# Kernel optimization log

Measured on AMD Instinct MI355X. Metric: run time of the kernel, lower is better.

The kernel has to match this reference:

```python
import jax, jax.numpy as jnp
import numpy as np

N_NODES = 32
GAT_OUT = 64
LSTM_H = 128
N_CLS = 4
NEG_SLOPE = 0.2


def setup_inputs() -> dict:
    key = jax.random.key(0)
    ks = jax.random.split(key, 12)
    B, T, E = 32, 512, 96
    F, H = GAT_OUT, LSTM_H
    s = 0.05
    return {
        "x_seq": jax.random.normal(ks[0], (B, T, N_NODES), jnp.float32),
        "edge_index": jax.random.randint(ks[1], (2, E), 0, N_NODES, jnp.int32),
        # GATConv params (heads=1): lin weight [in=1, F], attention vectors [F], bias [F]
        "w_gat": jax.random.normal(ks[2], (1, F), jnp.float32) * s,
        "att_src": jax.random.normal(ks[3], (F,), jnp.float32) * s,
        "att_dst": jax.random.normal(ks[4], (F,), jnp.float32) * s,
        "b_gat": jnp.zeros((F,), jnp.float32),
        # LSTM params, torch gate order (i, f, g, o)
        "W_ih": jax.random.normal(ks[5], (N_NODES * F, 4 * H), jnp.float32) * s,
        "W_hh": jax.random.normal(ks[6], (H, 4 * H), jnp.float32) * s,
        "b_ih": jnp.zeros((4 * H,), jnp.float32),
        "b_hh": jnp.zeros((4 * H,), jnp.float32),
        # classifier
        "W_fc": jax.random.normal(ks[7], (H, N_CLS), jnp.float32) * s,
        "b_fc": jnp.zeros((N_CLS,), jnp.float32),
    }


def _forward(x_seq, edge_index, w_gat, att_src, att_dst, b_gat,
             W_ih, W_hh, b_ih, b_hh, W_fc, b_fc):
    B, T, N = x_seq.shape
    F = w_gat.shape[1]
    H = W_hh.shape[0]

    # --- GAT over all (B,T) steps at once (PyG GATConv, heads=1, self-loops) ---
    loops = jnp.arange(N, dtype=edge_index.dtype)
    src = jnp.concatenate([edge_index[0], loops])  # [Et]
    dst = jnp.concatenate([edge_index[1], loops])  # [Et]
    Et = src.shape[0]

    h = x_seq[..., None] * w_gat            # [B,T,N,F] (in_channels=1 linear)
    a_s = h @ att_src                        # [B,T,N]
    a_d = h @ att_dst                        # [B,T,N]
    e = a_s[..., src] + a_d[..., dst]        # [B,T,Et]
    e = jnp.where(e > 0, e, NEG_SLOPE * e)   # LeakyReLU(0.2)

    # segment softmax over destination node, batched over B*T
    e2 = jnp.moveaxis(e, -1, 0).reshape(Et, B * T)
    m = jax.ops.segment_max(e2, dst, num_segments=N)        # [N,B*T]
    ex = jnp.exp(e2 - m[dst])
    z = jax.ops.segment_sum(ex, dst, num_segments=N)        # [N,B*T]
    alpha = ex / z[dst]                                      # [Et,B*T]
    alpha = jnp.moveaxis(alpha.reshape(Et, B, T), 0, -1)     # [B,T,Et]

    msg = alpha[..., None] * h[:, :, src, :]                 # [B,T,Et,F]
    onehot = (dst[:, None] == jnp.arange(N)).astype(h.dtype)  # [Et,N]
    out = jnp.einsum('btef,en->btnf', msg, onehot) + b_gat    # [B,T,N,F]

    seq = out.reshape(B, T, N * F)           # [B,T,2048]

    # --- single-layer LSTM (batch_first), torch gate order i,f,g,o ---
    xw = seq @ W_ih + (b_ih + b_hh)          # [B,T,4H]

    def step(carry, xw_t):
        hs, cs = carry
        g = xw_t + hs @ W_hh                 # [B,4H]
        i, f, gg, o = jnp.split(g, 4, axis=-1)
        cs = jax.nn.sigmoid(f) * cs + jax.nn.sigmoid(i) * jnp.tanh(gg)
        hs = jax.nn.sigmoid(o) * jnp.tanh(cs)
        return (hs, cs), None

    h0 = jnp.zeros((B, H), seq.dtype)
    (h_last, _), _ = jax.lax.scan(step, (h0, h0), jnp.moveaxis(xw, 1, 0))

    return h_last @ W_fc + b_fc              # [B,num_classes]


def reference(x_seq, edge_index, w_gat, att_src, att_dst, b_gat,
              W_ih, W_hh, b_ih, b_hh, W_fc, b_fc):
    return _forward(x_seq, edge_index, w_gat, att_src, att_dst, b_gat,
                    W_ih, W_hh, b_ih, b_hh, W_fc, b_fc)
```

## Files before the change

kernel.cpp:

```cpp
#include <hip/hip_runtime.h>

#define NN 32
#define FF 64
#define HH 128
#define G4 512
#define BB 32
#define TT 512
#define ET 128
#define NPOS (BB*TT)
#define POSB 32

__device__ __forceinline__ float frcp(float x) { return __builtin_amdgcn_rcpf(x); }

__global__ __launch_bounds__(512) void prep_kernel(const float* __restrict__ w_gat,
                                                   const float* __restrict__ b_gat,
                                                   const float* __restrict__ W_ih,
                                                   const float* __restrict__ W_hh,
                                                   float* __restrict__ W_eff,
                                                   float* __restrict__ biasp,
                                                   float* __restrict__ Wt) {
  int j = threadIdx.x;
  int n = blockIdx.x;
  float accw = 0.f, accb = 0.f;
#pragma unroll 8
  for (int f = 0; f < FF; ++f) {
    float wv = W_ih[(n * FF + f) * G4 + j];
    accw = fmaf(w_gat[f], wv, accw);
    accb = fmaf(b_gat[f], wv, accb);
  }
  W_eff[n * G4 + j] = accw;
  biasp[n * G4 + j] = accb;
  int g0 = (n * G4 + j) * 4;
#pragma unroll
  for (int q = 0; q < 4; ++q) {
    int e = g0 + q;
    int tl = e >> 7, idx = e & 127;
    int r = tl >> 2, kq = tl & 3;
    int g = idx >> 5, kk = idx & 31;
    Wt[e] = W_hh[(kq * 32 + kk) * G4 + g * 128 + r];
  }
}

__global__ __launch_bounds__(256) void gatxw_kernel(const float* __restrict__ x_seq,
                                                    const int* __restrict__ ei,
                                                    const float* __restrict__ w_gat,
                                                    const float* __restrict__ att_src,
                                                    const float* __restrict__ att_dst,
                                                    const float* __restrict__ b_ih,
                                                    const float* __restrict__ b_hh,
                                                    const float* __restrict__ W_eff,
                                                    const float* __restrict__ biasp,
                                                    float* __restrict__ xw) {
  __shared__ int srt[ET];
  __shared__ int offs[NN + 1];
  __shared__ int cnt[NN];
  __shared__ float xs[POSB * NN];
  __shared__ float sl[POSB * NN];
  __shared__ float scal_sh[2];
  int tid = threadIdx.x;
  int posbase = blockIdx.x * POSB;
  float we0[NN], we1[NN];
#pragma unroll
  for (int nn = 0; nn < NN; ++nn) {
    we0[nn] = W_eff[nn * G4 + tid];
    we1[nn] = W_eff[nn * G4 + 256 + tid];
  }
  float b0 = b_ih[tid] + b_hh[tid];
  float b1 = b_ih[256 + tid] + b_hh[256 + tid];
#pragma unroll 8
  for (int n = 0; n < NN; ++n) {
    b0 += biasp[n * G4 + tid];
    b1 += biasp[n * G4 + 256 + tid];
  }
  if (tid < NN) cnt[tid] = 0;
  __syncthreads();
  int es = 0, ed = 0, tk = 0;
  if (tid < ET) {
    if (tid < 96) { es = ei[tid]; ed = ei[96 + tid]; }
    else { es = tid - 96; ed = tid - 96; }
    tk = atomicAdd(&cnt[ed], 1);
  }
  __syncthreads();
  if (tid == 0) {
    offs[0] = 0;
    for (int n = 0; n < NN; ++n) offs[n + 1] = offs[n] + cnt[n];
  }
  if (tid == 1) {
    float cs = 0.f, cd = 0.f;
    for (int f = 0; f < FF; ++f) {
      cs = fmaf(w_gat[f], att_src[f], cs);
      cd = fmaf(w_gat[f], att_dst[f], cd);
    }
    scal_sh[0] = cs;
    scal_sh[1] = cd;
  }
  __syncthreads();
  if (tid < ET) srt[offs[ed] + tk] = es;
#pragma unroll
  for (int c = 0; c < POSB * NN / 256; ++c)
    xs[c * 256 + tid] = x_seq[posbase * NN + c * 256 + tid];
  __syncthreads();
  float cs = scal_sh[0], cd = scal_sh[1];
  int n = tid & 31;
  int e0 = offs[n], e1 = offs[n + 1];
#pragma unroll
  for (int pb = 0; pb < POSB / 8; ++pb) {
    int p = pb * 8 + (tid >> 5);
    int base = p * 32;
    float xn = xs[base + n];
    float cdxn = cd * xn;
    float m = -3.0e38f;
    for (int e = e0; e < e1; ++e) {
      float ev = fmaf(cs, xs[base + srt[e]], cdxn);
      ev = ev > 0.f ? ev : 0.2f * ev;
      m = fmaxf(m, ev);
    }
    float z = 0.f, sa = 0.f;
    for (int e = e0; e < e1; ++e) {
      float xsv = xs[base + srt[e]];
      float ev = fmaf(cs, xsv, cdxn);
      ev = ev > 0.f ? ev : 0.2f * ev;
      float ex = __expf(ev - m);
      z += ex;
      sa = fmaf(ex, xsv, sa);
    }
    sl[base + n] = sa * frcp(z);
  }
  __syncthreads();
#pragma unroll 4
  for (int pp = 0; pp < POSB; ++pp) {
    const float4* sp = (const float4*)&sl[pp * 32];
    float a0 = b0, a1 = b1;
#pragma unroll
    for (int q = 0; q < 8; ++q) {
      float4 sv = sp[q];
      a0 = fmaf(sv.x, we0[4 * q], a0);
      a0 = fmaf(sv.y, we0[4 * q + 1], a0);
      a0 = fmaf(sv.z, we0[4 * q + 2], a0);
      a0 = fmaf(sv.w, we0[4 * q + 3], a0);
      a1 = fmaf(sv.x, we1[4 * q], a1);
      a1 = fmaf(sv.y, we1[4 * q + 1], a1);
      a1 = fmaf(sv.z, we1[4 * q + 2], a1);
      a1 = fmaf(sv.w, we1[4 * q + 3], a1);
    }
    size_t row = (size_t)(posbase + pp) * G4;
    xw[row + tid] = a0;
    xw[row + 256 + tid] = a1;
  }
}


#define PK16F(HP, W0, W1, W2, W3) \
  "v_pk_fma_f32 v[216:217], v[" HP "], v[" W0 "], 0\n\t" \
  "v_pk_fma_f32 v[218:219], v[" HP "], v[" W1 "], 0\n\t" \
  "v_pk_fma_f32 v[220:221], v[" HP "], v[" W2 "], 0\n\t" \
  "v_pk_fma_f32 v[222:223], v[" HP "], v[" W3 "], 0\n\t"

#define PK16A(HP, W0, W1, W2, W3) \
  "v_pk_fma_f32 v[216:217], v[" HP "], v[" W0 "], v[216:217]\n\t" \
  "v_pk_fma_f32 v[218:219], v[" HP "], v[" W1 "], v[218:219]\n\t" \
  "v_pk_fma_f32 v[220:221], v[" HP "], v[" W2 "], v[220:221]\n\t" \
  "v_pk_fma_f32 v[222:223], v[" HP "], v[" W3 "], v[222:223]\n\t"

#define PHASE(XSLOT, RD, WR) \
  "ds_read_b128 v[32:35], " RD "\n\t" \
  "ds_read_b128 v[36:39], " RD " offset:16\n\t" \
  "ds_read_b128 v[40:43], " RD " offset:32\n\t" \
  "ds_read_b128 v[44:47], " RD " offset:48\n\t" \
  "ds_read_b128 v[48:51], " RD " offset:64\n\t" \
  "ds_read_b128 v[52:55], " RD " offset:80\n\t" \
  "ds_read_b128 v[56:59], " RD " offset:96\n\t" \
  "ds_read_b128 v[60:63], " RD " offset:112\n\t" \
  "s_waitcnt lgkmcnt(7)\n\t" \
  PK16F("32:33", "64:65",  "96:97",   "128:129", "160:161") \
  PK16A("34:35", "66:67",  "98:99",   "130:131", "162:163") \
  "s_waitcnt lgkmcnt(6)\n\t" \
  PK16A("36:37", "68:69",  "100:101", "132:133", "164:165") \
  PK16A("38:39", "70:71",  "102:103", "134:135", "166:167") \
  "s_waitcnt lgkmcnt(5)\n\t" \
  PK16A("40:41", "72:73",  "104:105", "136:137", "168:169") \
  PK16A("42:43", "74:75",  "106:107", "138:139", "170:171") \
  "s_waitcnt lgkmcnt(4)\n\t" \
  PK16A("44:45", "76:77",  "108:109", "140:141", "172:173") \
  PK16A("46:47", "78:79",  "110:111", "142:143", "174:175") \
  "s_waitcnt lgkmcnt(3)\n\t" \
  PK16A("48:49", "80:81",  "112:113", "144:145", "176:177") \
  PK16A("50:51", "82:83",  "114:115", "146:147", "178:179") \
  "s_waitcnt lgkmcnt(2)\n\t" \
  PK16A("52:53", "84:85",  "116:117", "148:149", "180:181") \
  PK16A("54:55", "86:87",  "118:119", "150:151", "182:183") \
  "s_waitcnt lgkmcnt(1)\n\t" \
  PK16A("56:57", "88:89",  "120:121", "152:153", "184:185") \
  PK16A("58:59", "90:91",  "122:123", "154:155", "186:187") \
  "s_waitcnt lgkmcnt(0)\n\t" \
  PK16A("60:61", "92:93",  "124:125", "156:157", "188:189") \
  PK16A("62:63", "94:95",  "126:127", "158:159", "190:191") \
  "s_waitcnt vmcnt(3)\n\t" \
  "v_mov_b32 v215, " XSLOT "\n\t" \
  "global_load_dword " XSLOT ", v194, %[xwb]\n\t" \
  "v_add_u32 v194, 0x800, v194\n\t" \
  "v_add_f32 v204, v216, v217\n\t" \
  "v_add_f32 v205, v218, v219\n\t" \
  "v_add_f32 v206, v220, v221\n\t" \
  "v_add_f32 v207, v222, v223\n\t" \
  "v_add_f32_dpp v204, v204, v204 quad_perm:[1,0,3,2] row_mask:0xf bank_mask:0xf\n\t" \
  "v_add_f32_dpp v205, v205, v205 quad_perm:[1,0,3,2] row_mask:0xf bank_mask:0xf\n\t" \
  "v_add_f32_dpp v206, v206, v206 quad_perm:[1,0,3,2] row_mask:0xf bank_mask:0xf\n\t" \
  "v_add_f32_dpp v207, v207, v207 quad_perm:[1,0,3,2] row_mask:0xf bank_mask:0xf\n\t" \
  "v_add_f32_dpp v204, v204, v204 quad_perm:[2,3,0,1] row_mask:0xf bank_mask:0xf\n\t" \
  "v_add_f32_dpp v205, v205, v205 quad_perm:[2,3,0,1] row_mask:0xf bank_mask:0xf\n\t" \
  "v_add_f32_dpp v206, v206, v206 quad_perm:[2,3,0,1] row_mask:0xf bank_mask:0xf\n\t" \
  "v_add_f32_dpp v207, v207, v207 quad_perm:[2,3,0,1] row_mask:0xf bank_mask:0xf\n\t" \
  "v_cndmask_b32 v208, v204, v205, s[22:23]\n\t" \
  "v_cndmask_b32 v209, v206, v207, s[22:23]\n\t" \
  "v_cndmask_b32 v208, v208, v209, s[24:25]\n\t" \
  "v_add_f32 v208, v208, v215\n\t" \
  "v_mul_f32 v209, v200, v208\n\t" \
  "v_exp_f32 v209, v209\n\t" \
  "s_nop 0\n\t" \
  "v_add_f32 v209, 1.0, v209\n\t" \
  "v_rcp_f32 v209, v209\n\t" \
  "s_nop 0\n\t" \
  "v_fma_f32 v210, v201, v209, v202\n\t" \
  "s_nop 1\n\t" \
  "v_add_f32_dpp v211, v210, v203 quad_perm:[0,0,0,0] row_mask:0xf bank_mask:0xf\n\t" \
  "v_add_f32_dpp v212, v210, v203 quad_perm:[1,1,1,1] row_mask:0xf bank_mask:0xf\n\t" \
  "v_add_f32_dpp v213, v210, v203 quad_perm:[2,2,2,2] row_mask:0xf bank_mask:0xf\n\t" \
  "v_add_f32_dpp v214, v210, v203 quad_perm:[3,3,3,3] row_mask:0xf bank_mask:0xf\n\t" \
  "v_mul_f32 v211, v211, v213\n\t" \
  "v_fma_f32 v199, v212, v199, v211\n\t" \
  "v_mul_f32 v209, 0x4038aa3b, v199\n\t" \
  "v_exp_f32 v209, v209\n\t" \
  "s_nop 0\n\t" \
  "v_add_f32 v209, 1.0, v209\n\t" \
  "v_rcp_f32 v209, v209\n\t" \
  "s_nop 0\n\t" \
  "v_fma_f32 v209, -2.0, v209, 1.0\n\t" \
  "v_mul_f32 v209, v214, v209\n\t" \
  "ds_write_b32 " WR ", v209\n\t" \
  "s_waitcnt lgkmcnt(0)\n\t" \
  "s_barrier\n\t"

__global__ __launch_bounds__(512, 2) void lstm_kernel(const float* __restrict__ xw,
                                                      const float* __restrict__ Wt,
                                                      const float* __restrict__ W_fc,
                                                      const float* __restrict__ b_fc,
                                                      float* __restrict__ out) {
  __shared__ __align__(16) float lds[320];
  int b = blockIdx.x, tid = threadIdx.x;
  int r = tid >> 2, kq = tid & 3;
  if (tid < 320) lds[tid] = 0.f;
  const float* xwb = xw + (size_t)b * TT * G4;
  unsigned xoff0 = (unsigned)((kq * 128 + r) * 4);
  unsigned wtoff = (unsigned)(tid * 512);
  unsigned lbase = (unsigned)(uintptr_t)&lds[0];
  unsigned rda = lbase + kq * 160;
  unsigned rdb = rda + 640;
  unsigned wra = lbase + (((r >> 5) * 40 + (r & 31)) << 2);
  unsigned wrb = wra + 640;
  float kmulf = (kq == 2) ? __uint_as_float(0x4038aa3bu)
                          : __uint_as_float(0xbfb8aa3bu);
  float Af = (kq == 2) ? -2.f : 1.f;
  float Bf = (kq == 2) ? 1.f : 0.f;
  unsigned kqodd = kq & 1, kqhi = kq >> 1;
  __syncthreads();
  asm volatile(
    "v_mov_b32 v194, %[xo]\n\t"
    "v_mov_b32 v195, %[rda]\n\t"
    "v_mov_b32 v196, %[rdb]\n\t"
    "v_mov_b32 v197, %[wra]\n\t"
    "v_mov_b32 v198, %[wrb]\n\t"
    "v_mov_b32 v199, 0\n\t"
    "v_mov_b32 v200, %[km]\n\t"
    "v_mov_b32 v201, %[Aa]\n\t"
    "v_mov_b32 v202, %[Bb]\n\t"
    "v_mov_b32 v203, 0\n\t"
    "v_cmp_eq_u32 s[22:23], 1, %[kodd]\n\t"
    "v_cmp_eq_u32 s[24:25], 1, %[khi]\n\t"
    "global_load_dword v224, v194, %[xwb]\n\t"
    "v_add_u32 v194, 0x800, v194\n\t"
    "global_load_dword v225, v194, %[xwb]\n\t"
    "v_add_u32 v194, 0x800, v194\n\t"
    "global_load_dword v226, v194, %[xwb]\n\t"
    "v_add_u32 v194, 0x800, v194\n\t"
    "global_load_dword v227, v194, %[xwb]\n\t"
    "v_add_u32 v194, 0x800, v194\n\t"
    "global_load_dwordx4 v[64:67], %[wto], %[wtb] offset:0\n\t"
    "global_load_dwordx4 v[68:71], %[wto], %[wtb] offset:16\n\t"
    "global_load_dwordx4 v[72:75], %[wto], %[wtb] offset:32\n\t"
    "global_load_dwordx4 v[76:79], %[wto], %[wtb] offset:48\n\t"
    "global_load_dwordx4 v[80:83], %[wto], %[wtb] offset:64\n\t"
    "global_load_dwordx4 v[84:87], %[wto], %[wtb] offset:80\n\t"
    "global_load_dwordx4 v[88:91], %[wto], %[wtb] offset:96\n\t"
    "global_load_dwordx4 v[92:95], %[wto], %[wtb] offset:112\n\t"
    "global_load_dwordx4 v[96:99], %[wto], %[wtb] offset:128\n\t"
    "global_load_dwordx4 v[100:103], %[wto], %[wtb] offset:144\n\t"
    "global_load_dwordx4 v[104:107], %[wto], %[wtb] offset:160\n\t"
    "global_load_dwordx4 v[108:111], %[wto], %[wtb] offset:176\n\t"
    "global_load_dwordx4 v[112:115], %[wto], %[wtb] offset:192\n\t"
    "global_load_dwordx4 v[116:119], %[wto], %[wtb] offset:208\n\t"
    "global_load_dwordx4 v[120:123], %[wto], %[wtb] offset:224\n\t"
    "global_load_dwordx4 v[124:127], %[wto], %[wtb] offset:240\n\t"
    "global_load_dwordx4 v[128:131], %[wto], %[wtb] offset:256\n\t"
    "global_load_dwordx4 v[132:135], %[wto], %[wtb] offset:272\n\t"
    "global_load_dwordx4 v[136:139], %[wto], %[wtb] offset:288\n\t"
    "global_load_dwordx4 v[140:143], %[wto], %[wtb] offset:304\n\t"
    "global_load_dwordx4 v[144:147], %[wto], %[wtb] offset:320\n\t"
    "global_load_dwordx4 v[148:151], %[wto], %[wtb] offset:336\n\t"
    "global_load_dwordx4 v[152:155], %[wto], %[wtb] offset:352\n\t"
    "global_load_dwordx4 v[156:159], %[wto], %[wtb] offset:368\n\t"
    "global_load_dwordx4 v[160:163], %[wto], %[wtb] offset:384\n\t"
    "global_load_dwordx4 v[164:167], %[wto], %[wtb] offset:400\n\t"
    "global_load_dwordx4 v[168:171], %[wto], %[wtb] offset:416\n\t"
    "global_load_dwordx4 v[172:175], %[wto], %[wtb] offset:432\n\t"
    "global_load_dwordx4 v[176:179], %[wto], %[wtb] offset:448\n\t"
    "global_load_dwordx4 v[180:183], %[wto], %[wtb] offset:464\n\t"
    "global_load_dwordx4 v[184:187], %[wto], %[wtb] offset:480\n\t"
    "global_load_dwordx4 v[188:191], %[wto], %[wtb] offset:496\n\t"
    "s_waitcnt vmcnt(0)\n\t"
    "s_movk_i32 s20, 0x80\n\t"
    "L_lstm_%=:\n\t"
    PHASE("v224", "v195", "v198")
    PHASE("v225", "v196", "v197")
    PHASE("v226", "v195", "v198")
    PHASE("v227", "v196", "v197")
    "s_sub_u32 s20, s20, 1\n\t"
    "s_cmp_lg_u32 s20, 0\n\t"
    "s_cbranch_scc1 L_lstm_%=\n\t"
    "s_waitcnt vmcnt(0) lgkmcnt(0)\n\t"
    :
    : [xwb]"s"(xwb), [wtb]"s"(Wt), [wto]"v"(wtoff), [xo]"v"(xoff0),
      [rda]"v"(rda), [rdb]"v"(rdb), [wra]"v"(wra), [wrb]"v"(wrb),
      [km]"v"(kmulf), [Aa]"v"(Af), [Bb]"v"(Bf),
      [kodd]"v"(kqodd), [khi]"v"(kqhi)
    : "memory", "scc", "s20", "s22", "s23", "s24", "s25",
      "v32","v33","v34","v35","v36","v37","v38","v39",
      "v40","v41","v42","v43","v44","v45","v46","v47",
      "v48","v49","v50","v51","v52","v53","v54","v55",
      "v56","v57","v58","v59","v60","v61","v62","v63",
      "v64","v65","v66","v67","v68","v69","v70","v71",
      "v72","v73","v74","v75","v76","v77","v78","v79",
      "v80","v81","v82","v83","v84","v85","v86","v87",
      "v88","v89","v90","v91","v92","v93","v94","v95",
      "v96","v97","v98","v99","v100","v101","v102","v103",
      "v104","v105","v106","v107","v108","v109","v110","v111",
      "v112","v113","v114","v115","v116","v117","v118","v119",
      "v120","v121","v122","v123","v124","v125","v126","v127",
      "v128","v129","v130","v131","v132","v133","v134","v135",
      "v136","v137","v138","v139","v140","v141","v142","v143",
      "v144","v145","v146","v147","v148","v149","v150","v151",
      "v152","v153","v154","v155","v156","v157","v158","v159",
      "v160","v161","v162","v163","v164","v165","v166","v167",
      "v168","v169","v170","v171","v172","v173","v174","v175",
      "v176","v177","v178","v179","v180","v181","v182","v183",
      "v184","v185","v186","v187","v188","v189","v190","v191",
      "v192","v193","v194","v195","v196","v197","v198","v199",
      "v200","v201","v202","v203","v204","v205","v206","v207",
      "v208","v209","v210","v211","v212","v213","v214","v215",
      "v216","v217","v218","v219","v220","v221","v222","v223",
      "v224","v225","v226","v227");
  __syncthreads();
  if (tid < 4) {
    float acc = b_fc[tid];
#pragma unroll 8
    for (int k = 0; k < HH; ++k)
      acc = fmaf(lds[(k >> 5) * 40 + (k & 31)], W_fc[k * 4 + tid], acc);
    out[b * 4 + tid] = acc;
  }
}

extern "C" void kernel_launch(void* const* d_in, const int* in_sizes, int n_in,
                              void* d_out, int out_size, void* d_ws, size_t ws_size,
                              hipStream_t stream) {
  const float* x_seq   = (const float*)d_in[0];
  const int*   ei      = (const int*)d_in[1];
  const float* w_gat   = (const float*)d_in[2];
  const float* att_src = (const float*)d_in[3];
  const float* att_dst = (const float*)d_in[4];
  const float* b_gat   = (const float*)d_in[5];
  const float* W_ih    = (const float*)d_in[6];
  const float* W_hh    = (const float*)d_in[7];
  const float* b_ih    = (const float*)d_in[8];
  const float* b_hh    = (const float*)d_in[9];
  const float* W_fc    = (const float*)d_in[10];
  const float* b_fc    = (const float*)d_in[11];

  float* ws = (float*)d_ws;
  float* Wt    = ws;
  float* xw    = Wt + 65536;
  float* W_eff = xw + (size_t)(NPOS + 8) * G4;
  float* biasp = W_eff + NN * G4;

  prep_kernel<<<NN, G4, 0, stream>>>(w_gat, b_gat, W_ih, W_hh, W_eff, biasp, Wt);
  gatxw_kernel<<<NPOS / POSB, 256, 0, stream>>>(x_seq, ei, w_gat, att_src, att_dst,
                                                b_ih, b_hh, W_eff, biasp, xw);
  lstm_kernel<<<BB, G4, 0, stream>>>(xw, Wt, W_fc, b_fc, (float*)d_out);
}
```

Baseline: 374.7 us.

## Use fp16 dot2 for LSTM recurrent matvec with half-precision weights and hidden state

Stores the transposed W_hh in fp16, packed so that consecutive k pairs sit together, and stores the hidden state in LDS as fp16. The recurrent matvec then uses v_dot2_f32_f16 with fp32 accumulation in place of packed fp32 FMAs. This halves the per-step LDS reads and the register-resident weight footprint, and drops the pairwise add stage before the DPP reduction. The cost is lower precision in the recurrence over 512 steps, which risks numerical drift.

```diff
diff --git a/kernel.cpp b/kernel.cpp
--- a/kernel.cpp
+++ b/kernel.cpp
@@ -1,4 +1,5 @@
 #include <hip/hip_runtime.h>
+#include <hip/hip_fp16.h>
 
 #define NN 32
 #define FF 64
@@ -30,14 +31,18 @@
   }
   W_eff[n * G4 + j] = accw;
   biasp[n * G4 + j] = accb;
+  __half* Wt16 = (__half*)Wt;
   int g0 = (n * G4 + j) * 4;
 #pragma unroll
   for (int q = 0; q < 4; ++q) {
-    int e = g0 + q;
-    int tl = e >> 7, idx = e & 127;
+    int E = g0 + q;
+    int tl = E >> 7, idx = E & 127;
     int r = tl >> 2, kq = tl & 3;
-    int g = idx >> 5, kk = idx & 31;
-    Wt[e] = W_hh[(kq * 32 + kk) * G4 + g * 128 + r];
+    int P = idx >> 3;
+    int g = (idx >> 1) & 3;
+    int e = idx & 1;
+    int k = kq * 32 + 2 * P + e;
+    Wt16[E] = __float2half(W_hh[k * G4 + g * 128 + r]);
   }
 }
 
@@ -150,70 +155,58 @@
 }
 
 
-#define PK16F(HP, W0, W1, W2, W3) \
-  "v_pk_fma_f32 v[216:217], v[" HP "], v[" W0 "], 0\n\t" \
-  "v_pk_fma_f32 v[218:219], v[" HP "], v[" W1 "], 0\n\t" \
-  "v_pk_fma_f32 v[220:221], v[" HP "], v[" W2 "], 0\n\t" \
-  "v_pk_fma_f32 v[222:223], v[" HP "], v[" W3 "], 0\n\t"
-
-#define PK16A(HP, W0, W1, W2, W3) \
-  "v_pk_fma_f32 v[216:217], v[" HP "], v[" W0 "], v[216:217]\n\t" \
-  "v_pk_fma_f32 v[218:219], v[" HP "], v[" W1 "], v[218:219]\n\t" \
-  "v_pk_fma_f32 v[220:221], v[" HP "], v[" W2 "], v[220:221]\n\t" \
-  "v_pk_fma_f32 v[222:223], v[" HP "], v[" W3 "], v[222:223]\n\t"
+#define D2F(HJ, W0, W1, W2, W3) \
+  "v_dot2_f32_f16 v216, v" HJ ", v" W0 ", 0\n\t" \
+  "v_dot2_f32_f16 v217, v" HJ ", v" W1 ", 0\n\t" \
+  "v_dot2_f32_f16 v218, v" HJ ", v" W2 ", 0\n\t" \
+  "v_dot2_f32_f16 v219, v" HJ ", v" W3 ", 0\n\t"
+
+#define D2A(HJ, W0, W1, W2, W3) \
+  "v_dot2_f32_f16 v216, v" HJ ", v" W0 ", v216\n\t" \
+  "v_dot2_f32_f16 v217, v" HJ ", v" W1 ", v217\n\t" \
+  "v_dot2_f32_f16 v218, v" HJ ", v" W2 ", v218\n\t" \
+  "v_dot2_f32_f16 v219, v" HJ ", v" W3 ", v219\n\t"
 
 #define PHASE(XSLOT, RD, WR) \
   "ds_read_b128 v[32:35], " RD "\n\t" \
   "ds_read_b128 v[36:39], " RD " offset:16\n\t" \
   "ds_read_b128 v[40:43], " RD " offset:32\n\t" \
   "ds_read_b128 v[44:47], " RD " offset:48\n\t" \
-  "ds_read_b128 v[48:51], " RD " offset:64\n\t" \
-  "ds_read_b128 v[52:55], " RD " offset:80\n\t" \
-  "ds_read_b128 v[56:59], " RD " offset:96\n\t" \
-  "ds_read_b128 v[60:63], " RD " offset:112\n\t" \
-  "s_waitcnt lgkmcnt(7)\n\t" \
-  PK16F("32:33", "64:65",  "96:97",   "128:129", "160:161") \
-  PK16A("34:35", "66:67",  "98:99",   "130:131", "162:163") \
-  "s_waitcnt lgkmcnt(6)\n\t" \
-  PK16A("36:37", "68:69",  "100:101", "132:133", "164:165") \
-  PK16A("38:39", "70:71",  "102:103", "134:135", "166:167") \
-  "s_waitcnt lgkmcnt(5)\n\t" \
-  PK16A("40:41", "72:73",  "104:105", "136:137", "168:169") \
-  PK16A("42:43", "74:75",  "106:107", "138:139", "170:171") \
-  "s_waitcnt lgkmcnt(4)\n\t" \
-  PK16A("44:45", "76:77",  "108:109", "140:141", "172:173") \
-  PK16A("46:47", "78:79",  "110:111", "142:143", "174:175") \
   "s_waitcnt lgkmcnt(3)\n\t" \
-  PK16A("48:49", "80:81",  "112:113", "144:145", "176:177") \
-  PK16A("50:51", "82:83",  "114:115", "146:147", "178:179") \
+  D2F("32", "64", "65", "66", "67") \
+  D2A("33", "68", "69", "70", "71") \
+  D2A("34", "72", "73", "74", "75") \
+  D2A("35", "76", "77", "78", "79") \
   "s_waitcnt lgkmcnt(2)\n\t" \
-  PK16A("52:53", "84:85",  "116:117", "148:149", "180:181") \
-  PK16A("54:55", "86:87",  "118:119", "150:151", "182:183") \
+  D2A("36", "80", "81", "82", "83") \
+  D2A("37", "84", "85", "86", "87") \
+  D2A("38", "88", "89", "90", "91") \
+  D2A("39", "92", "93", "94", "95") \
   "s_waitcnt lgkmcnt(1)\n\t" \
-  PK16A("56:57", "88:89",  "120:121", "152:153", "184:185") \
-  PK16A("58:59", "90:91",  "122:123", "154:155", "186:187") \
+  D2A("40", "96", "97", "98", "99") \
+  D2A("41", "100", "101", "102", "103") \
+  D2A("42", "104", "105", "106", "107") \
+  D2A("43", "108", "109", "110", "111") \
   "s_waitcnt lgkmcnt(0)\n\t" \
-  PK16A("60:61", "92:93",  "124:125", "156:157", "188:189") \
-  PK16A("62:63", "94:95",  "126:127", "158:159", "190:191") \
+  D2A("44", "112", "113", "114", "115") \
+  D2A("45", "116", "117", "118", "119") \
+  D2A("46", "120", "121", "122", "123") \
+  D2A("47", "124", "125", "126", "127") \
+  "v_add_f32_dpp v216, v216, v216 quad_perm:[1,0,3,2] row_mask:0xf bank_mask:0xf\n\t" \
+  "v_add_f32_dpp v217, v217, v217 quad_perm:[1,0,3,2] row_mask:0xf bank_mask:0xf\n\t" \
+  "v_add_f32_dpp v218, v218, v218 quad_perm:[1,0,3,2] row_mask:0xf bank_mask:0xf\n\t" \
+  "v_add_f32_dpp v219, v219, v219 quad_perm:[1,0,3,2] row_mask:0xf bank_mask:0xf\n\t" \
+  "v_add_f32_dpp v216, v216, v216 quad_perm:[2,3,0,1] row_mask:0xf bank_mask:0xf\n\t" \
+  "v_add_f32_dpp v217, v217, v217 quad_perm:[2,3,0,1] row_mask:0xf bank_mask:0xf\n\t" \
+  "v_add_f32_dpp v218, v218, v218 quad_perm:[2,3,0,1] row_mask:0xf bank_mask:0xf\n\t" \
+  "v_add_f32_dpp v219, v219, v219 quad_perm:[2,3,0,1] row_mask:0xf bank_mask:0xf\n\t" \
+  "v_cndmask_b32 v208, v216, v217, s[22:23]\n\t" \
+  "v_cndmask_b32 v209, v218, v219, s[22:23]\n\t" \
+  "v_cndmask_b32 v208, v208, v209, s[24:25]\n\t" \
   "s_waitcnt vmcnt(3)\n\t" \
   "v_mov_b32 v215, " XSLOT "\n\t" \
   "global_load_dword " XSLOT ", v194, %[xwb]\n\t" \
   "v_add_u32 v194, 0x800, v194\n\t" \
-  "v_add_f32 v204, v216, v217\n\t" \
-  "v_add_f32 v205, v218, v219\n\t" \
-  "v_add_f32 v206, v220, v221\n\t" \
-  "v_add_f32 v207, v222, v223\n\t" \
-  "v_add_f32_dpp v204, v204, v204 quad_perm:[1,0,3,2] row_mask:0xf bank_mask:0xf\n\t" \
-  "v_add_f32_dpp v205, v205, v205 quad_perm:[1,0,3,2] row_mask:0xf bank_mask:0xf\n\t" \
-  "v_add_f32_dpp v206, v206, v206 quad_perm:[1,0,3,2] row_mask:0xf bank_mask:0xf\n\t" \
-  "v_add_f32_dpp v207, v207, v207 quad_perm:[1,0,3,2] row_mask:0xf bank_mask:0xf\n\t" \
-  "v_add_f32_dpp v204, v204, v204 quad_perm:[2,3,0,1] row_mask:0xf bank_mask:0xf\n\t" \
-  "v_add_f32_dpp v205, v205, v205 quad_perm:[2,3,0,1] row_mask:0xf bank_mask:0xf\n\t" \
-  "v_add_f32_dpp v206, v206, v206 quad_perm:[2,3,0,1] row_mask:0xf bank_mask:0xf\n\t" \
-  "v_add_f32_dpp v207, v207, v207 quad_perm:[2,3,0,1] row_mask:0xf bank_mask:0xf\n\t" \
-  "v_cndmask_b32 v208, v204, v205, s[22:23]\n\t" \
-  "v_cndmask_b32 v209, v206, v207, s[22:23]\n\t" \
-  "v_cndmask_b32 v208, v208, v209, s[24:25]\n\t" \
   "v_add_f32 v208, v208, v215\n\t" \
   "v_mul_f32 v209, v200, v208\n\t" \
   "v_exp_f32 v209, v209\n\t" \
@@ -237,7 +230,8 @@
   "s_nop 0\n\t" \
   "v_fma_f32 v209, -2.0, v209, 1.0\n\t" \
   "v_mul_f32 v209, v214, v209\n\t" \
-  "ds_write_b32 " WR ", v209\n\t" \
+  "v_cvt_f16_f32 v209, v209\n\t" \
+  "ds_write_b16 " WR ", v209\n\t" \
   "s_waitcnt lgkmcnt(0)\n\t" \
   "s_barrier\n\t"
 
@@ -246,18 +240,18 @@
                                                       const float* __restrict__ W_fc,
                                                       const float* __restrict__ b_fc,
                                                       float* __restrict__ out) {
-  __shared__ __align__(16) float lds[320];
+  __shared__ __align__(16) float lds[160];
   int b = blockIdx.x, tid = threadIdx.x;
   int r = tid >> 2, kq = tid & 3;
-  if (tid < 320) lds[tid] = 0.f;
+  if (tid < 160) lds[tid] = 0.f;
   const float* xwb = xw + (size_t)b * TT * G4;
   unsigned xoff0 = (unsigned)((kq * 128 + r) * 4);
-  unsigned wtoff = (unsigned)(tid * 512);
+  unsigned wtoff = (unsigned)(tid * 256);
   unsigned lbase = (unsigned)(uintptr_t)&lds[0];
-  unsigned rda = lbase + kq * 160;
-  unsigned rdb = rda + 640;
-  unsigned wra = lbase + (((r >> 5) * 40 + (r & 31)) << 2);
-  unsigned wrb = wra + 640;
+  unsigned rda = lbase + (unsigned)(kq * 80);
+  unsigned rdb = rda + 320;
+  unsigned wra = lbase + (unsigned)(((r >> 5) * 40 + (r & 31)) * 2);
+  unsigned wrb = wra + 320;
   float kmulf = (kq == 2) ? __uint_as_float(0x4038aa3bu)
                           : __uint_as_float(0xbfb8aa3bu);
   float Af = (kq == 2) ? -2.f : 1.f;
@@ -301,22 +295,6 @@
     "global_load_dwordx4 v[116:119], %[wto], %[wtb] offset:208\n\t"
     "global_load_dwordx4 v[120:123], %[wto], %[wtb] offset:224\n\t"
     "global_load_dwordx4 v[124:127], %[wto], %[wtb] offset:240\n\t"
-    "global_load_dwordx4 v[128:131], %[wto], %[wtb] offset:256\n\t"
-    "global_load_dwordx4 v[132:135], %[wto], %[wtb] offset:272\n\t"
-    "global_load_dwordx4 v[136:139], %[wto], %[wtb] offset:288\n\t"
-    "global_load_dwordx4 v[140:143], %[wto], %[wtb] offset:304\n\t"
-    "global_load_dwordx4 v[144:147], %[wto], %[wtb] offset:320\n\t"
-    "global_load_dwordx4 v[148:151], %[wto], %[wtb] offset:336\n\t"
-    "global_load_dwordx4 v[152:155], %[wto], %[wtb] offset:352\n\t"
-    "global_load_dwordx4 v[156:159], %[wto], %[wtb] offset:368\n\t"
-    "global_load_dwordx4 v[160:163], %[wto], %[wtb] offset:384\n\t"
-    "global_load_dwordx4 v[164:167], %[wto], %[wtb] offset:400\n\t"
-    "global_load_dwordx4 v[168:171], %[wto], %[wtb] offset:416\n\t"
-    "global_load_dwordx4 v[172:175], %[wto], %[wtb] offset:432\n\t"
-    "global_load_dwordx4 v[176:179], %[wto], %[wtb] offset:448\n\t"
-    "global_load_dwordx4 v[180:183], %[wto], %[wtb] offset:464\n\t"
-    "global_load_dwordx4 v[184:187], %[wto], %[wtb] offset:480\n\t"
-    "global_load_dwordx4 v[188:191], %[wto], %[wtb] offset:496\n\t"
     "s_waitcnt vmcnt(0)\n\t"
     "s_movk_i32 s20, 0x80\n\t"
     "L_lstm_%=:\n\t"
@@ -336,8 +314,6 @@
     : "memory", "scc", "s20", "s22", "s23", "s24", "s25",
       "v32","v33","v34","v35","v36","v37","v38","v39",
       "v40","v41","v42","v43","v44","v45","v46","v47",
-      "v48","v49","v50","v51","v52","v53","v54","v55",
-      "v56","v57","v58","v59","v60","v61","v62","v63",
       "v64","v65","v66","v67","v68","v69","v70","v71",
       "v72","v73","v74","v75","v76","v77","v78","v79",
       "v80","v81","v82","v83","v84","v85","v86","v87",
@@ -346,25 +322,18 @@
       "v104","v105","v106","v107","v108","v109","v110","v111",
       "v112","v113","v114","v115","v116","v117","v118","v119",
       "v120","v121","v122","v123","v124","v125","v126","v127",
-      "v128","v129","v130","v131","v132","v133","v134","v135",
-      "v136","v137","v138","v139","v140","v141","v142","v143",
-      "v144","v145","v146","v147","v148","v149","v150","v151",
-      "v152","v153","v154","v155","v156","v157","v158","v159",
-      "v160","v161","v162","v163","v164","v165","v166","v167",
-      "v168","v169","v170","v171","v172","v173","v174","v175",
-      "v176","v177","v178","v179","v180","v181","v182","v183",
-      "v184","v185","v186","v187","v188","v189","v190","v191",
-      "v192","v193","v194","v195","v196","v197","v198","v199",
+      "v194","v195","v196","v197","v198","v199",
       "v200","v201","v202","v203","v204","v205","v206","v207",
       "v208","v209","v210","v211","v212","v213","v214","v215",
-      "v216","v217","v218","v219","v220","v221","v222","v223",
+      "v216","v217","v218","v219",
       "v224","v225","v226","v227");
   __syncthreads();
   if (tid < 4) {
+    const __half* hf = (const __half*)lds;
     float acc = b_fc[tid];
 #pragma unroll 8
     for (int k = 0; k < HH; ++k)
-      acc = fmaf(lds[(k >> 5) * 40 + (k & 31)], W_fc[k * 4 + tid], acc);
+      acc = fmaf(__half2float(hf[(k >> 5) * 40 + (k & 31)]), W_fc[k * 4 + tid], acc);
     out[b * 4 + tid] = acc;
   }
 }
```

New measurement: 357.3 us. 1.05x faster.
